# Performance work log

Hardware: AMD Instinct MI355X
Metric: run time of the kernel (lower is better)

Reference implementation:

```python
import jax, jax.numpy as jnp
import numpy as np

B, A, D = 4, 2048, 512
HEADS = 4
HD = D // HEADS
EPS = 1e-5


def layernorm(x, w, b):
    mu = jnp.mean(x, axis=-1, keepdims=True)
    var = jnp.var(x, axis=-1, keepdims=True)
    return (x - mu) * jax.lax.rsqrt(var + EPS) * w + b


def swish(x):
    return x * jax.nn.sigmoid(x)


def setup_inputs() -> dict:
    key = jax.random.key(0)
    ks = jax.random.split(key, 8)
    s = 1.0 / np.sqrt(D)
    x = jax.random.normal(ks[0], (B, A, D), dtype=jnp.float32)
    conn = jax.random.bernoulli(ks[1], 0.05, (B, 1, A, A))
    eye = jnp.eye(A, dtype=bool)[None, None]
    connectivity = jnp.logical_or(conn, eye)
    Wq = jax.random.uniform(ks[2], (D, D), jnp.float32, -s, s)
    Wk = jax.random.uniform(ks[3], (D, D), jnp.float32, -s, s)
    Wv = jax.random.uniform(ks[4], (D, D), jnp.float32, -s, s)
    fc1_w = jax.random.uniform(ks[5], (D, D), jnp.float32, -s, s)
    fc2_w = jax.random.uniform(ks[6], (D, D), jnp.float32, -s, s)
    kb = jax.random.split(ks[7], 2)
    fc1_b = jax.random.uniform(kb[0], (D,), jnp.float32, -s, s)
    fc2_b = jax.random.uniform(kb[1], (D,), jnp.float32, -s, s)
    return {
        "x": x, "connectivity": connectivity,
        "Wq": Wq, "Wk": Wk, "Wv": Wv,
        "norm_w": jnp.ones((D,), jnp.float32), "norm_b": jnp.zeros((D,), jnp.float32),
        "ln1_w": jnp.ones((D,), jnp.float32), "ln1_b": jnp.zeros((D,), jnp.float32),
        "fc1_w": fc1_w, "fc1_b": fc1_b,
        "ln2_w": jnp.ones((D,), jnp.float32), "ln2_b": jnp.zeros((D,), jnp.float32),
        "fc2_w": fc2_w, "fc2_b": fc2_b,
    }


def reference(x, connectivity, Wq, Wk, Wv, norm_w, norm_b,
              ln1_w, ln1_b, fc1_w, fc1_b, ln2_w, ln2_b, fc2_w, fc2_b):
    xb, xa, _ = x.shape
    xn = layernorm(x, norm_w, norm_b)  # self.norm applied to input
    # [B,A,D] -> [B,H,A,hd]
    def split_heads(t):
        return t.reshape(xb, xa, HEADS, HD).transpose(0, 2, 1, 3)
    Q = split_heads(xn @ Wq.T)
    K = split_heads(xn @ Wk.T)
    V = split_heads(xn @ Wv.T)
    # PyTorch SDPA default scale = 1/sqrt(head_dim); self.scale is unused
    scores = jnp.einsum("bhqd,bhkd->bhqk", Q, K) / np.sqrt(HD)
    scores = jnp.where(connectivity, scores, -jnp.inf)
    attn = jax.nn.softmax(scores, axis=-1)
    out = jnp.einsum("bhqk,bhkd->bhqd", attn, V)
    out = out.transpose(0, 2, 1, 3).reshape(xb, xa, HEADS * HD)
    # forward_proj: Swish -> LN -> Linear -> Swish -> LN -> Linear
    h = layernorm(swish(out), ln1_w, ln1_b) @ fc1_w.T + fc1_b
    h = layernorm(swish(h), ln2_w, ln2_b) @ fc2_w.T + fc2_b
    return layernorm(h, norm_w, norm_b)  # same self.norm instance again
```

## Files before the change

### kernel.cpp

```cpp
#include <hip/hip_runtime.h>
#include <cstdint>
#include <cstddef>

#define A_LEN  2048
#define D_DIM  512
#define NHEADS 4
#define HDIM   128
#define B_SZ   4
#define ROWS   8192
#define LN_EPS 1e-5f
#define KSPLIT 2
#define KCHUNK (A_LEN / KSPLIT)
#define KTILE  32
#define QBLK   128

typedef __bf16 bf16x8 __attribute__((ext_vector_type(8)));
typedef __bf16 bf16x4 __attribute__((ext_vector_type(4)));
typedef float  f32x4  __attribute__((ext_vector_type(4)));
typedef float  f32x16 __attribute__((ext_vector_type(16)));
typedef unsigned int uint32x2 __attribute__((ext_vector_type(2)));

#define GLOAD_LDS(g, l) __builtin_amdgcn_global_load_lds(                      \
    (__attribute__((address_space(1))) const void*)(const void*)(g),           \
    (__attribute__((address_space(3))) void*)(void*)(l), 16, 0, 0)

static __device__ __forceinline__ uint32_t pkbf(float a, float b) {
    union { __bf16 h[2]; uint32_t u; } t;
    t.h[0] = (__bf16)a; t.h[1] = (__bf16)b;
    return t.u;
}

__global__ __launch_bounds__(256) void ln_kernel(
    const void* __restrict__ in, void* __restrict__ out,
    const float* __restrict__ w, const float* __restrict__ bvec,
    int do_swish, int in_bf16, int out_bf16)
{
    int row  = blockIdx.x * 4 + (threadIdx.x >> 6);
    int lane = threadIdx.x & 63;
    float v[8];
    if (in_bf16) {
        bf16x8 iv = *(const bf16x8*)((const __bf16*)in + (size_t)row * D_DIM + lane * 8);
#pragma unroll
        for (int j = 0; j < 8; ++j) v[j] = (float)iv[j];
    } else {
        const float* x = (const float*)in + (size_t)row * D_DIM + lane * 8;
        float4 a  = *(const float4*)x;
        float4 b4 = *(const float4*)(x + 4);
        v[0]=a.x; v[1]=a.y; v[2]=a.z; v[3]=a.w;
        v[4]=b4.x; v[5]=b4.y; v[6]=b4.z; v[7]=b4.w;
    }
    if (do_swish) {
#pragma unroll
        for (int j = 0; j < 8; ++j) v[j] = v[j] / (1.f + __expf(-v[j]));
    }
    float s = 0.f, s2 = 0.f;
#pragma unroll
    for (int j = 0; j < 8; ++j) { s += v[j]; s2 += v[j] * v[j]; }
#pragma unroll
    for (int off = 32; off; off >>= 1) {
        s  += __shfl_xor(s,  off);
        s2 += __shfl_xor(s2, off);
    }
    float mean = s * (1.f / D_DIM);
    float var  = s2 * (1.f / D_DIM) - mean * mean;
    float inv  = rsqrtf(var + LN_EPS);
    const float* wp = w + lane * 8;
    const float* bp = bvec + lane * 8;
    float r[8];
#pragma unroll
    for (int j = 0; j < 8; ++j) r[j] = (v[j] - mean) * inv * wp[j] + bp[j];
    if (out_bf16) {
        bf16x8 ov;
#pragma unroll
        for (int j = 0; j < 8; ++j) ov[j] = (__bf16)r[j];
        *(bf16x8*)((__bf16*)out + (size_t)row * D_DIM + lane * 8) = ov;
    } else {
        float* o = (float*)out + (size_t)row * D_DIM + lane * 8;
        float4 o0 = {r[0], r[1], r[2], r[3]}, o1 = {r[4], r[5], r[6], r[7]};
        *(float4*)o = o0; *(float4*)(o + 4) = o1;
    }
}

__global__ __launch_bounds__(256) void conv_w5_kernel(
    const float* __restrict__ s0, const float* __restrict__ s1,
    const float* __restrict__ s2, const float* __restrict__ s3,
    const float* __restrict__ s4, __bf16* __restrict__ dst)
{
    int widx = blockIdx.y;
    const float* src = widx == 0 ? s0 : widx == 1 ? s1 : widx == 2 ? s2
                     : widx == 3 ? s3 : s4;
    size_t i = ((size_t)blockIdx.x * 256 + threadIdx.x) * 8;
    float4 a = *(const float4*)(src + i);
    float4 b = *(const float4*)(src + i + 4);
    bf16x8 o;
    o[0]=(__bf16)a.x; o[1]=(__bf16)a.y; o[2]=(__bf16)a.z; o[3]=(__bf16)a.w;
    o[4]=(__bf16)b.x; o[5]=(__bf16)b.y; o[6]=(__bf16)b.z; o[7]=(__bf16)b.w;
    *(bf16x8*)(dst + (size_t)widx * D_DIM * D_DIM + i) = o;
}

__global__ __launch_bounds__(256) void mask_pack_kernel(
    const int* __restrict__ conn, uint32_t* __restrict__ mpt)
{
    size_t i = (size_t)blockIdx.x * 256 + threadIdx.x;
    uint64_t bal = __ballot(conn[i] != 0);
    int lane = threadIdx.x & 63;
    int b  = (int)(i >> 22);
    int q  = (int)((i >> 11) & (A_LEN - 1));
    int k0 = (int)(i & (A_LEN - 1) & ~(size_t)63);
    if (lane == 0)
        mpt[((size_t)b * 64 + (k0 >> 5)) * A_LEN + q] = (uint32_t)bal;
    else if (lane == 1)
        mpt[((size_t)b * 64 + (k0 >> 5) + 1) * A_LEN + q] = (uint32_t)(bal >> 32);
}

#define GBM 128
#define GBK 32
#define GPAD 40

__global__ __launch_bounds__(256) void gemm_qkv(
    const __bf16* __restrict__ Am, const __bf16* __restrict__ Wall,
    __bf16* __restrict__ Qh, __bf16* __restrict__ Kh, __bf16* __restrict__ Vt2)
{
    const int K = D_DIM;
    __shared__ alignas(16) __bf16 As[2][GBM][GPAD];
    __shared__ alignas(16) __bf16 Ws[2][GBM][GPAD];
    int tid = threadIdx.x;
    int w = tid >> 6, lane = tid & 63;
    int grp = lane >> 4, col = lane & 15;
    int wr = w >> 1, wc = w & 1;
    int m0 = blockIdx.x * GBM;
    int widx = blockIdx.y >> 2;
    int h    = blockIdx.y & 3;
    const __bf16* Wm = Wall + (size_t)widx * D_DIM * D_DIM;
    int n0 = h * 128;

    int srow = tid >> 1;
    int skc  = (tid & 1) * 16;
    const __bf16* agp = Am + (size_t)(m0 + srow) * K + skc;
    const __bf16* wgp = Wm + (size_t)(n0 + srow) * K + skc;

    uint4 ar0, ar1, wr0, wr1;
    ar0 = *(const uint4*)agp;       ar1 = *(const uint4*)(agp + 8);
    wr0 = *(const uint4*)wgp;       wr1 = *(const uint4*)(wgp + 8);
    *(uint4*)&As[0][srow][skc] = ar0; *(uint4*)&As[0][srow][skc + 8] = ar1;
    *(uint4*)&Ws[0][srow][skc] = wr0; *(uint4*)&Ws[0][srow][skc + 8] = wr1;
    __syncthreads();

    f32x4 acc[4][4] = {};
#pragma unroll 1
    for (int t = 0; t < K / GBK; ++t) {
        int cur = t & 1;
        bool more = (t + 1) < K / GBK;
        if (more) {
            const __bf16* ap = agp + (size_t)(t + 1) * GBK;
            const __bf16* wp = wgp + (size_t)(t + 1) * GBK;
            ar0 = *(const uint4*)ap; ar1 = *(const uint4*)(ap + 8);
            wr0 = *(const uint4*)wp; wr1 = *(const uint4*)(wp + 8);
        }
        bf16x8 af[4], wf[4];
#pragma unroll
        for (int mt = 0; mt < 4; ++mt)
            af[mt] = *(const bf16x8*)&As[cur][wr * 64 + mt * 16 + col][grp * 8];
#pragma unroll
        for (int nt = 0; nt < 4; ++nt)
            wf[nt] = *(const bf16x8*)&Ws[cur][wc * 64 + nt * 16 + col][grp * 8];
        __builtin_amdgcn_s_setprio(1);
#pragma unroll
        for (int mt = 0; mt < 4; ++mt)
#pragma unroll
            for (int nt = 0; nt < 4; ++nt)
                acc[mt][nt] = __builtin_amdgcn_mfma_f32_16x16x32_bf16(
                    af[mt], wf[nt], acc[mt][nt], 0, 0, 0);
        __builtin_amdgcn_s_setprio(0);
        if (more) {
            int nb = cur ^ 1;
            *(uint4*)&As[nb][srow][skc] = ar0; *(uint4*)&As[nb][srow][skc + 8] = ar1;
            *(uint4*)&Ws[nb][srow][skc] = wr0; *(uint4*)&Ws[nb][srow][skc + 8] = wr1;
        }
        __syncthreads();
    }

    const float QSCALE = 0.08838834764831845f;
    if (widx == 2) {
#pragma unroll
        for (int mt = 0; mt < 4; ++mt) {
            int m = m0 + wr * 64 + mt * 16 + grp * 4;
            int b = m >> 11, a = m & (A_LEN - 1);
            int kt = a >> 5, k32 = a & 31;
            int bh = b * NHEADS + h;
#pragma unroll
            for (int nt = 0; nt < 4; ++nt) {
                int d = wc * 64 + nt * 16 + col;
                bf16x4 o;
                o[0] = (__bf16)acc[mt][nt][0]; o[1] = (__bf16)acc[mt][nt][1];
                o[2] = (__bf16)acc[mt][nt][2]; o[3] = (__bf16)acc[mt][nt][3];
                *(bf16x4*)(Vt2 + (((size_t)bh * 64 + kt) * HDIM + d) * 32 + k32) = o;
            }
        }
    } else {
        __bf16* Cb = widx == 0 ? Qh : Kh;
        float sc = widx == 0 ? QSCALE : 1.0f;
#pragma unroll
        for (int nt = 0; nt < 4; ++nt) {
            int d = wc * 64 + nt * 16 + col;
#pragma unroll
            for (int mt = 0; mt < 4; ++mt) {
#pragma unroll
                for (int r = 0; r < 4; ++r) {
                    int m = m0 + wr * 64 + mt * 16 + grp * 4 + r;
                    int b = m >> 11, a = m & (A_LEN - 1);
                    Cb[((size_t)(b * NHEADS + h) * A_LEN + a) * HDIM + d] =
                        (__bf16)(acc[mt][nt][r] * sc);
                }
            }
        }
    }
}

__global__ __launch_bounds__(256) void gemm_tile64(
    const __bf16* __restrict__ Am, const __bf16* __restrict__ Wm,
    const float* __restrict__ bias, __bf16* __restrict__ C)
{
    const int N = D_DIM, K = D_DIM;
    __shared__ alignas(16) __bf16 As[2][128][GPAD];
    __shared__ alignas(16) __bf16 Ws[2][64][GPAD];
    int tid = threadIdx.x;
    int w = tid >> 6, lane = tid & 63;
    int grp = lane >> 4, col = lane & 15;
    int m0 = blockIdx.x * 128;
    int n0 = blockIdx.y * 64;

    int srow = tid >> 1;
    int skc  = (tid & 1) * 16;
    int wrow = tid >> 2;
    int wkc  = (tid & 3) * 8;
    const __bf16* agp = Am + (size_t)(m0 + srow) * K + skc;
    const __bf16* wgp = Wm + (size_t)(n0 + wrow) * K + wkc;

    uint4 ar0, ar1, wv0;
    ar0 = *(const uint4*)agp;  ar1 = *(const uint4*)(agp + 8);
    wv0 = *(const uint4*)wgp;
    *(uint4*)&As[0][srow][skc] = ar0; *(uint4*)&As[0][srow][skc + 8] = ar1;
    *(uint4*)&Ws[0][wrow][wkc] = wv0;
    __syncthreads();

    f32x4 acc[2][4] = {};
#pragma unroll 1
    for (int t = 0; t < K / GBK; ++t) {
        int cur = t & 1;
        bool more = (t + 1) < K / GBK;
        if (more) {
            const __bf16* ap = agp + (size_t)(t + 1) * GBK;
            const __bf16* wp = wgp + (size_t)(t + 1) * GBK;
            ar0 = *(const uint4*)ap; ar1 = *(const uint4*)(ap + 8);
            wv0 = *(const uint4*)wp;
        }
        bf16x8 af[2], wf[4];
#pragma unroll
        for (int mt = 0; mt < 2; ++mt)
            af[mt] = *(const bf16x8*)&As[cur][w * 32 + mt * 16 + col][grp * 8];
#pragma unroll
        for (int nt = 0; nt < 4; ++nt)
            wf[nt] = *(const bf16x8*)&Ws[cur][nt * 16 + col][grp * 8];
        __builtin_amdgcn_s_setprio(1);
#pragma unroll
        for (int mt = 0; mt < 2; ++mt)
#pragma unroll
            for (int nt = 0; nt < 4; ++nt)
                acc[mt][nt] = __builtin_amdgcn_mfma_f32_16x16x32_bf16(
                    af[mt], wf[nt], acc[mt][nt], 0, 0, 0);
        __builtin_amdgcn_s_setprio(0);
        if (more) {
            int nb = cur ^ 1;
            *(uint4*)&As[nb][srow][skc] = ar0; *(uint4*)&As[nb][srow][skc + 8] = ar1;
            *(uint4*)&Ws[nb][wrow][wkc] = wv0;
        }
        __syncthreads();
    }

#pragma unroll
    for (int nt = 0; nt < 4; ++nt) {
        int n = n0 + nt * 16 + col;
        float bv = bias[n];
#pragma unroll
        for (int mt = 0; mt < 2; ++mt) {
#pragma unroll
            for (int r = 0; r < 4; ++r) {
                int m = m0 + w * 32 + mt * 16 + grp * 4 + r;
                C[(size_t)m * N + n] = (__bf16)(acc[mt][nt][r] + bv);
            }
        }
    }
}

__global__ __launch_bounds__(256, 2) void attn_mfma(
    const __bf16* __restrict__ Qh, const __bf16* __restrict__ Kh,
    const __bf16* __restrict__ Vt2, const uint32_t* __restrict__ MPT,
    __bf16* __restrict__ Opart, float* __restrict__ lsum)
{
    int flat = blockIdx.x;
    int swz  = (flat & 7) * 64 + (flat >> 3);
    int qx    = swz & 15;
    int bh    = (swz >> 4) & 15;
    int split = swz >> 8;
    int b = bh >> 2;
    int ks0 = split * KCHUNK;
    int tid = threadIdx.x;
    int w = tid >> 6, lane = tid & 63;
    int c31 = lane & 31, hi = lane >> 5;
    int qw = qx * QBLK + w * 32;

    __shared__ alignas(16) __bf16 Klds[2][KTILE][128];
    __shared__ alignas(16) __bf16 Vlds[2][HDIM][32];

    bf16x8 qf[8];
    {
        const __bf16* qptr = Qh + ((size_t)bh * A_LEN + qw + c31) * HDIM + hi * 8;
#pragma unroll
        for (int s = 0; s < 8; ++s) qf[s] = *(const bf16x8*)(qptr + s * 16);
    }

    const __bf16* Ksrc = Kh + ((size_t)bh * A_LEN + ks0) * HDIM;
    const __bf16* Vsrc = Vt2 + ((size_t)bh * 64 + (ks0 >> 5)) * HDIM * 32;
    const uint32_t* mpq = MPT + ((size_t)b * 64 + (ks0 >> 5)) * A_LEN + qw + c31;
    int kxor = c31 & 15;
    int vxor = c31 & 3;

    int krow0 = w * 4 + (lane >> 4);
    int kso0  = krow0 * HDIM + (((lane & 15) ^ (krow0 & 15)) * 8);
    int krow1 = (4 + w) * 4 + (lane >> 4);
    int kso1  = krow1 * HDIM + (((lane & 15) ^ (krow1 & 15)) * 8);
    int vd0   = w * 16 + (lane >> 2);
    int vso0  = vd0 * 32 + (((lane & 3) ^ (vd0 & 3)) * 8);
    int vd1   = (4 + w) * 16 + (lane >> 2);
    int vso1  = vd1 * 32 + (((lane & 3) ^ (vd1 & 3)) * 8);

    float l_part = 0.f;
    f32x16 oacc[4];
#pragma unroll
    for (int dt = 0; dt < 4; ++dt)
#pragma unroll
        for (int j = 0; j < 16; ++j) oacc[dt][j] = 0.f;

    {
        __bf16* kb = &Klds[0][0][0];
        __bf16* vb = &Vlds[0][0][0];
        GLOAD_LDS(Ksrc + kso0, kb + (size_t)w * 512);
        GLOAD_LDS(Ksrc + kso1, kb + (size_t)(4 + w) * 512);
        GLOAD_LDS(Vsrc + vso0, vb + (size_t)w * 512);
        GLOAD_LDS(Vsrc + vso1, vb + (size_t)(4 + w) * 512);
    }
    __syncthreads();

    const int ntl = KCHUNK / KTILE;
#pragma unroll 1
    for (int t = 0; t < ntl; ++t) {
        int cur = t & 1;
        bool more = (t + 1) < ntl;
        if (more) {
            const __bf16* kp = Ksrc + (size_t)(t + 1) * KTILE * HDIM;
            const __bf16* vp = Vsrc + (size_t)(t + 1) * HDIM * 32;
            __bf16* kb = &Klds[cur ^ 1][0][0];
            __bf16* vb = &Vlds[cur ^ 1][0][0];
            GLOAD_LDS(kp + kso0, kb + (size_t)w * 512);
            GLOAD_LDS(kp + kso1, kb + (size_t)(4 + w) * 512);
            GLOAD_LDS(vp + vso0, vb + (size_t)w * 512);
            GLOAD_LDS(vp + vso1, vb + (size_t)(4 + w) * 512);
        }

        uint32_t mw = mpq[(size_t)t * A_LEN];

        f32x16 St;
#pragma unroll
        for (int j = 0; j < 16; ++j) St[j] = 0.f;
        __builtin_amdgcn_s_setprio(1);
#pragma unroll
        for (int s = 0; s < 8; ++s) {
            bf16x8 kf = *(const bf16x8*)&Klds[cur][c31][(((s << 1) | hi) ^ kxor) * 8];
            St = __builtin_amdgcn_mfma_f32_32x32x16_bf16(kf, qf[s], St, 0, 0, 0);
        }
        __builtin_amdgcn_s_setprio(0);

#pragma unroll
        for (int r = 0; r < 16; ++r) {
            int kb = (r & 3) + 8 * (r >> 2) + 4 * hi;
            float e = __expf(St[r]);
            St[r] = ((mw >> kb) & 1u) ? e : 0.f;
            l_part += St[r];
        }

        bf16x8 pa[2];
#pragma unroll
        for (int sub = 0; sub < 2; ++sub) {
            uint32_t pk01 = pkbf(St[sub*8+0], St[sub*8+1]);
            uint32_t pk23 = pkbf(St[sub*8+2], St[sub*8+3]);
            uint32_t pk45 = pkbf(St[sub*8+4], St[sub*8+5]);
            uint32_t pk67 = pkbf(St[sub*8+6], St[sub*8+7]);
            uint32x2 e0 = __builtin_amdgcn_permlane32_swap(pk01, pk45, false, false);
            uint32x2 e1 = __builtin_amdgcn_permlane32_swap(pk23, pk67, false, false);
            union { uint32_t u[4]; bf16x8 v; } fu;
            fu.u[0] = e0[0];
            fu.u[1] = e1[0];
            fu.u[2] = e0[1];
            fu.u[3] = e1[1];
            pa[sub] = fu.v;
        }

        __builtin_amdgcn_s_setprio(1);
#pragma unroll
        for (int dt = 0; dt < 4; ++dt) {
            const __bf16* vrow = &Vlds[cur][dt * 32 + c31][0];
            bf16x8 v0 = *(const bf16x8*)(vrow + ((hi)     ^ vxor) * 8);
            bf16x8 v1 = *(const bf16x8*)(vrow + ((2 | hi) ^ vxor) * 8);
            oacc[dt] = __builtin_amdgcn_mfma_f32_32x32x16_bf16(pa[0], v0, oacc[dt], 0, 0, 0);
            oacc[dt] = __builtin_amdgcn_mfma_f32_32x32x16_bf16(pa[1], v1, oacc[dt], 0, 0, 0);
        }
        __builtin_amdgcn_s_setprio(0);

        __syncthreads();
    }

    float l_tot = l_part + __shfl_xor(l_part, 32);
    if (lane < 32)
        lsum[((size_t)split * 16 + bh) * A_LEN + qw + lane] = l_tot;

    __bf16* ob = Opart + (((size_t)split * 16 + bh) * A_LEN + qw) * HDIM;
#pragma unroll
    for (int r = 0; r < 16; ++r) {
        int ql = (r & 3) + 8 * (r >> 2) + 4 * hi;
#pragma unroll
        for (int dt = 0; dt < 4; ++dt)
            ob[(size_t)ql * HDIM + dt * 32 + c31] = (__bf16)oacc[dt][r];
    }
}

__global__ __launch_bounds__(256) void attn_merge_ln(
    const __bf16* __restrict__ Opart, const float* __restrict__ lsum,
    const float* __restrict__ lw, const float* __restrict__ lb,
    __bf16* __restrict__ xbout)
{
    int wv = threadIdx.x >> 6, lane = threadIdx.x & 63;
    int ridx = blockIdx.x * 4 + wv;
    int b = ridx >> 11, a = ridx & (A_LEN - 1);
    int d512 = lane * 8;
    int h = d512 >> 7, d = d512 & 127;
    int bh = b * NHEADS + h;

    float l0 = lsum[(size_t)bh * A_LEN + a];
    float l1 = lsum[((size_t)16 + bh) * A_LEN + a];
    float inv = 1.f / (l0 + l1);

    bf16x8 v0 = *(const bf16x8*)(Opart + ((size_t)bh * A_LEN + a) * HDIM + d);
    bf16x8 v1 = *(const bf16x8*)(Opart + (((size_t)16 + bh) * A_LEN + a) * HDIM + d);
    float v[8];
#pragma unroll
    for (int j = 0; j < 8; ++j) {
        float o = ((float)v0[j] + (float)v1[j]) * inv;
        v[j] = o / (1.f + __expf(-o));
    }
    float s = 0.f, s2 = 0.f;
#pragma unroll
    for (int j = 0; j < 8; ++j) { s += v[j]; s2 += v[j] * v[j]; }
#pragma unroll
    for (int off = 32; off; off >>= 1) {
        s  += __shfl_xor(s,  off);
        s2 += __shfl_xor(s2, off);
    }
    float mean = s * (1.f / D_DIM);
    float var  = s2 * (1.f / D_DIM) - mean * mean;
    float rinv = rsqrtf(var + LN_EPS);
    bf16x8 ov;
#pragma unroll
    for (int j = 0; j < 8; ++j)
        ov[j] = (__bf16)((v[j] - mean) * rinv * lw[d512 + j] + lb[d512 + j]);
    *(bf16x8*)(xbout + (size_t)ridx * D_DIM + d512) = ov;
}

extern "C" void kernel_launch(void* const* d_in, const int* in_sizes, int n_in,
                              void* d_out, int out_size, void* d_ws, size_t ws_size,
                              hipStream_t stream)
{
    const float* x      = (const float*)d_in[0];
    const int*   conn   = (const int*)d_in[1];
    const float* Wq     = (const float*)d_in[2];
    const float* Wk     = (const float*)d_in[3];
    const float* Wv     = (const float*)d_in[4];
    const float* norm_w = (const float*)d_in[5];
    const float* norm_b = (const float*)d_in[6];
    const float* ln1_w  = (const float*)d_in[7];
    const float* ln1_b  = (const float*)d_in[8];
    const float* fc1_w  = (const float*)d_in[9];
    const float* fc1_b  = (const float*)d_in[10];
    const float* ln2_w  = (const float*)d_in[11];
    const float* ln2_b  = (const float*)d_in[12];
    const float* fc2_w  = (const float*)d_in[13];
    const float* fc2_b  = (const float*)d_in[14];
    float* out = (float*)d_out;

    char* wsb = (char*)d_ws;
    const size_t WELEM = (size_t)D_DIM * D_DIM;
    const size_t MB = (size_t)1 << 20;
    __bf16*   wall = (__bf16*)(wsb);
    uint32_t* mpt = (uint32_t*)(wsb + 3 * MB);
    float*    lsm = (float*)(wsb + 5 * MB);
    __bf16*   xb  = (__bf16*)(wsb + 6 * MB);
    __bf16*   Qh  = (__bf16*)(wsb + 14 * MB);
    __bf16*   Kh  = (__bf16*)(wsb + 22 * MB);
    __bf16*   Vt2 = (__bf16*)(wsb + 30 * MB);
    __bf16*   Op  = (__bf16*)(wsb + 38 * MB);
    __bf16*   h1  = (__bf16*)(wsb + 14 * MB);
    __bf16*   h2  = (__bf16*)(wsb + 22 * MB);

    dim3 blk(256);
    dim3 lnGrid(ROWS / 4);
    dim3 cwGrid(WELEM / 8 / 256, 5);
    dim3 qkvGrid(ROWS / GBM, 12);
    dim3 fcGrid(ROWS / 128, D_DIM / 64);
    dim3 attnGrid(16 * 16 * KSPLIT);
    dim3 mergeGrid(ROWS / 4);
    dim3 mpGrid((size_t)B_SZ * A_LEN * A_LEN / 256);

    conv_w5_kernel<<<cwGrid, blk, 0, stream>>>(Wq, Wk, Wv, fc1_w, fc2_w, wall);
    mask_pack_kernel<<<mpGrid, blk, 0, stream>>>(conn, mpt);

    ln_kernel<<<lnGrid, blk, 0, stream>>>(x, xb, norm_w, norm_b, 0, 0, 1);
    gemm_qkv<<<qkvGrid, blk, 0, stream>>>(xb, wall, Qh, Kh, Vt2);
    attn_mfma<<<attnGrid, blk, 0, stream>>>(Qh, Kh, Vt2, mpt, Op, lsm);
    attn_merge_ln<<<mergeGrid, blk, 0, stream>>>(Op, lsm, ln1_w, ln1_b, xb);
    gemm_tile64<<<fcGrid, blk, 0, stream>>>(xb, wall + 3 * WELEM, fc1_b, h1);
    ln_kernel<<<lnGrid, blk, 0, stream>>>(h1, xb, ln2_w, ln2_b, 1, 1, 1);
    gemm_tile64<<<fcGrid, blk, 0, stream>>>(xb, wall + 4 * WELEM, fc2_b, h2);
    ln_kernel<<<lnGrid, blk, 0, stream>>>(h2, out, norm_w, norm_b, 0, 1, 0);
}
```

Baseline: 150.3 us.

## Use direct global-to-LDS loads with XOR swizzle in GEMM kernels

```diff
diff --git a/kernel.cpp b/kernel.cpp
--- a/kernel.cpp
+++ b/kernel.cpp
@@ -115,15 +115,14 @@
 
 #define GBM 128
 #define GBK 32
-#define GPAD 40
 
 __global__ __launch_bounds__(256) void gemm_qkv(
     const __bf16* __restrict__ Am, const __bf16* __restrict__ Wall,
     __bf16* __restrict__ Qh, __bf16* __restrict__ Kh, __bf16* __restrict__ Vt2)
 {
     const int K = D_DIM;
-    __shared__ alignas(16) __bf16 As[2][GBM][GPAD];
-    __shared__ alignas(16) __bf16 Ws[2][GBM][GPAD];
+    __shared__ alignas(16) __bf16 As[2][GBM][32];
+    __shared__ alignas(16) __bf16 Ws[2][GBM][32];
     int tid = threadIdx.x;
     int w = tid >> 6, lane = tid & 63;
     int grp = lane >> 4, col = lane & 15;
@@ -134,16 +133,16 @@
     const __bf16* Wm = Wall + (size_t)widx * D_DIM * D_DIM;
     int n0 = h * 128;
 
-    int srow = tid >> 1;
-    int skc  = (tid & 1) * 16;
-    const __bf16* agp = Am + (size_t)(m0 + srow) * K + skc;
-    const __bf16* wgp = Wm + (size_t)(n0 + srow) * K + skc;
-
-    uint4 ar0, ar1, wr0, wr1;
-    ar0 = *(const uint4*)agp;       ar1 = *(const uint4*)(agp + 8);
-    wr0 = *(const uint4*)wgp;       wr1 = *(const uint4*)(wgp + 8);
-    *(uint4*)&As[0][srow][skc] = ar0; *(uint4*)&As[0][srow][skc + 8] = ar1;
-    *(uint4*)&Ws[0][srow][skc] = wr0; *(uint4*)&Ws[0][srow][skc + 8] = wr1;
+    int r0  = w * 32 + (lane >> 2);
+    int cs  = (((lane & 3) ^ ((r0 >> 1) & 3)) * 8);
+    const __bf16* agp = Am + (size_t)(m0 + r0) * K + cs;
+    const __bf16* wgp = Wm + (size_t)(n0 + r0) * K + cs;
+    int rsw = (col >> 1) & 3;
+
+    GLOAD_LDS(agp,                    &As[0][w * 32][0]);
+    GLOAD_LDS(agp + (size_t)16 * K,   &As[0][w * 32 + 16][0]);
+    GLOAD_LDS(wgp,                    &Ws[0][w * 32][0]);
+    GLOAD_LDS(wgp + (size_t)16 * K,   &Ws[0][w * 32 + 16][0]);
     __syncthreads();
 
     f32x4 acc[4][4] = {};
@@ -154,16 +153,19 @@
         if (more) {
             const __bf16* ap = agp + (size_t)(t + 1) * GBK;
             const __bf16* wp = wgp + (size_t)(t + 1) * GBK;
-            ar0 = *(const uint4*)ap; ar1 = *(const uint4*)(ap + 8);
-            wr0 = *(const uint4*)wp; wr1 = *(const uint4*)(wp + 8);
+            int nb = cur ^ 1;
+            GLOAD_LDS(ap,                  &As[nb][w * 32][0]);
+            GLOAD_LDS(ap + (size_t)16 * K, &As[nb][w * 32 + 16][0]);
+            GLOAD_LDS(wp,                  &Ws[nb][w * 32][0]);
+            GLOAD_LDS(wp + (size_t)16 * K, &Ws[nb][w * 32 + 16][0]);
         }
         bf16x8 af[4], wf[4];
 #pragma unroll
         for (int mt = 0; mt < 4; ++mt)
-            af[mt] = *(const bf16x8*)&As[cur][wr * 64 + mt * 16 + col][grp * 8];
+            af[mt] = *(const bf16x8*)&As[cur][wr * 64 + mt * 16 + col][(grp ^ rsw) * 8];
 #pragma unroll
         for (int nt = 0; nt < 4; ++nt)
-            wf[nt] = *(const bf16x8*)&Ws[cur][wc * 64 + nt * 16 + col][grp * 8];
+            wf[nt] = *(const bf16x8*)&Ws[cur][wc * 64 + nt * 16 + col][(grp ^ rsw) * 8];
         __builtin_amdgcn_s_setprio(1);
 #pragma unroll
         for (int mt = 0; mt < 4; ++mt)
@@ -172,11 +174,6 @@
                 acc[mt][nt] = __builtin_amdgcn_mfma_f32_16x16x32_bf16(
                     af[mt], wf[nt], acc[mt][nt], 0, 0, 0);
         __builtin_amdgcn_s_setprio(0);
-        if (more) {
-            int nb = cur ^ 1;
-            *(uint4*)&As[nb][srow][skc] = ar0; *(uint4*)&As[nb][srow][skc + 8] = ar1;
-            *(uint4*)&Ws[nb][srow][skc] = wr0; *(uint4*)&Ws[nb][srow][skc + 8] = wr1;
-        }
         __syncthreads();
     }
 
@@ -222,26 +219,25 @@
     const float* __restrict__ bias, __bf16* __restrict__ C)
 {
     const int N = D_DIM, K = D_DIM;
-    __shared__ alignas(16) __bf16 As[2][128][GPAD];
-    __shared__ alignas(16) __bf16 Ws[2][64][GPAD];
+    __shared__ alignas(16) __bf16 As[2][128][32];
+    __shared__ alignas(16) __bf16 Ws[2][64][32];
     int tid = threadIdx.x;
     int w = tid >> 6, lane = tid & 63;
     int grp = lane >> 4, col = lane & 15;
     int m0 = blockIdx.x * 128;
     int n0 = blockIdx.y * 64;
 
-    int srow = tid >> 1;
-    int skc  = (tid & 1) * 16;
-    int wrow = tid >> 2;
-    int wkc  = (tid & 3) * 8;
-    const __bf16* agp = Am + (size_t)(m0 + srow) * K + skc;
-    const __bf16* wgp = Wm + (size_t)(n0 + wrow) * K + wkc;
-
-    uint4 ar0, ar1, wv0;
-    ar0 = *(const uint4*)agp;  ar1 = *(const uint4*)(agp + 8);
-    wv0 = *(const uint4*)wgp;
-    *(uint4*)&As[0][srow][skc] = ar0; *(uint4*)&As[0][srow][skc + 8] = ar1;
-    *(uint4*)&Ws[0][wrow][wkc] = wv0;
+    int rA = w * 32 + (lane >> 2);
+    int csA = (((lane & 3) ^ ((rA >> 1) & 3)) * 8);
+    int rW = w * 16 + (lane >> 2);
+    int csW = (((lane & 3) ^ ((rW >> 1) & 3)) * 8);
+    const __bf16* agp = Am + (size_t)(m0 + rA) * K + csA;
+    const __bf16* wgp = Wm + (size_t)(n0 + rW) * K + csW;
+    int rsw = (col >> 1) & 3;
+
+    GLOAD_LDS(agp,                  &As[0][w * 32][0]);
+    GLOAD_LDS(agp + (size_t)16 * K, &As[0][w * 32 + 16][0]);
+    GLOAD_LDS(wgp,                  &Ws[0][w * 16][0]);
     __syncthreads();
 
     f32x4 acc[2][4] = {};
@@ -252,16 +248,18 @@
         if (more) {
             const __bf16* ap = agp + (size_t)(t + 1) * GBK;
             const __bf16* wp = wgp + (size_t)(t + 1) * GBK;
-            ar0 = *(const uint4*)ap; ar1 = *(const uint4*)(ap + 8);
-            wv0 = *(const uint4*)wp;
+            int nb = cur ^ 1;
+            GLOAD_LDS(ap,                  &As[nb][w * 32][0]);
+            GLOAD_LDS(ap + (size_t)16 * K, &As[nb][w * 32 + 16][0]);
+            GLOAD_LDS(wp,                  &Ws[nb][w * 16][0]);
         }
         bf16x8 af[2], wf[4];
 #pragma unroll
         for (int mt = 0; mt < 2; ++mt)
-            af[mt] = *(const bf16x8*)&As[cur][w * 32 + mt * 16 + col][grp * 8];
+            af[mt] = *(const bf16x8*)&As[cur][w * 32 + mt * 16 + col][(grp ^ rsw) * 8];
 #pragma unroll
         for (int nt = 0; nt < 4; ++nt)
-            wf[nt] = *(const bf16x8*)&Ws[cur][nt * 16 + col][grp * 8];
+            wf[nt] = *(const bf16x8*)&Ws[cur][nt * 16 + col][(grp ^ rsw) * 8];
         __builtin_amdgcn_s_setprio(1);
 #pragma unroll
         for (int mt = 0; mt < 2; ++mt)
@@ -270,11 +268,6 @@
                 acc[mt][nt] = __builtin_amdgcn_mfma_f32_16x16x32_bf16(
                     af[mt], wf[nt], acc[mt][nt], 0, 0, 0);
         __builtin_amdgcn_s_setprio(0);
-        if (more) {
-            int nb = cur ^ 1;
-            *(uint4*)&As[nb][srow][skc] = ar0; *(uint4*)&As[nb][srow][skc + 8] = ar1;
-            *(uint4*)&Ws[nb][wrow][wkc] = wv0;
-        }
         __syncthreads();
     }
 
@@ -324,16 +317,16 @@
     const __bf16* Vsrc = Vt2 + ((size_t)bh * 64 + (ks0 >> 5)) * HDIM * 32;
     const uint32_t* mpq = MPT + ((size_t)b * 64 + (ks0 >> 5)) * A_LEN + qw + c31;
     int kxor = c31 & 15;
-    int vxor = c31 & 3;
+    int vsw  = (c31 >> 1) & 3;
 
     int krow0 = w * 4 + (lane >> 4);
     int kso0  = krow0 * HDIM + (((lane & 15) ^ (krow0 & 15)) * 8);
     int krow1 = (4 + w) * 4 + (lane >> 4);
     int kso1  = krow1 * HDIM + (((lane & 15) ^ (krow1 & 15)) * 8);
     int vd0   = w * 16 + (lane >> 2);
-    int vso0  = vd0 * 32 + (((lane & 3) ^ (vd0 & 3)) * 8);
-    int vd1   = (4 + w) * 16 + (lane >> 2);
-    int vso1  = vd1 * 32 + (((lane & 3) ^ (vd1 & 3)) * 8);
+    int vcs   = (((lane & 3) ^ ((vd0 >> 1) & 3)) * 8);
+    int vso0  = vd0 * 32 + vcs;
+    int vso1  = (vd0 + 64) * 32 + vcs;
 
     float l_part = 0.f;
     f32x16 oacc[4];
@@ -410,8 +403,8 @@
 #pragma unroll
         for (int dt = 0; dt < 4; ++dt) {
             const __bf16* vrow = &Vlds[cur][dt * 32 + c31][0];
-            bf16x8 v0 = *(const bf16x8*)(vrow + ((hi)     ^ vxor) * 8);
-            bf16x8 v1 = *(const bf16x8*)(vrow + ((2 | hi) ^ vxor) * 8);
+            bf16x8 v0 = *(const bf16x8*)(vrow + ((hi)     ^ vsw) * 8);
+            bf16x8 v1 = *(const bf16x8*)(vrow + ((2 | hi) ^ vsw) * 8);
             oacc[dt] = __builtin_amdgcn_mfma_f32_32x32x16_bf16(pa[0], v0, oacc[dt], 0, 0, 0);
             oacc[dt] = __builtin_amdgcn_mfma_f32_32x32x16_bf16(pa[1], v1, oacc[dt], 0, 0, 0);
         }
```

Result: slower. 153.9 us (+2.4%).
